# Kernel optimization log

Hardware: AMD Instinct MI355X
Metric: run time of the kernel (lower is better)

The kernel has to match this reference:

```python
import jax, jax.numpy as jnp
import numpy as np

BATCH = 2
TIME_N = 196
SPACE_F = 8
D_MODEL = 768
N_HEADS = 12
D_STATE = 16
DT_RANK = 48  # ceil(768/16)
D_CONV = 4
SEQ = 1 + TIME_N * SPACE_F


def _ln(x, w, b, eps=1e-5):
    m = x.mean(-1, keepdims=True)
    v = ((x - m) ** 2).mean(-1, keepdims=True)
    return (x - m) * jax.lax.rsqrt(v + eps) * w + b


def _silu(x):
    return x * jax.nn.sigmoid(x)


def _causal_conv(x, w, b):
    # x: (B, L, d); depthwise causal conv1d, kernel D_CONV, padding left
    L = x.shape[1]
    xp = jnp.pad(x, ((0, 0), (D_CONV - 1, 0), (0, 0)))
    return sum(xp[:, k:k + L, :] * w[:, k] for k in range(D_CONV)) + b


def _ssm(u, delta, A, Bm, C, Dp):
    # u, delta: (B,L,d); A: (d,N); Bm, C: (B,L,N)
    dA = jnp.exp(delta[..., None] * A)                    # (B,L,d,N)
    dBu = (delta * u)[..., None] * Bm[:, :, None, :]      # (B,L,d,N)
    B, L, d, N = dA.shape

    def step(h, inp):
        a, bu = inp
        h = a * h + bu
        return h, h

    _, hs = jax.lax.scan(step, jnp.zeros((B, d, N), dA.dtype),
                         (dA.transpose(1, 0, 2, 3), dBu.transpose(1, 0, 2, 3)))
    return jnp.einsum('lbdn,bln->bld', hs, C) + u * Dp


def _mamba_dir(xp, z, conv_w, conv_b, xproj_w, dt_w, dt_b, A_log, Dp, flip):
    if flip:
        xp = xp[:, ::-1]
        z = z[:, ::-1]
    xc = _silu(_causal_conv(xp, conv_w, conv_b))
    x_dbl = xc @ xproj_w.T
    dt = x_dbl[..., :DT_RANK]
    Bm = x_dbl[..., DT_RANK:DT_RANK + D_STATE]
    C = x_dbl[..., DT_RANK + D_STATE:]
    delta = jax.nn.softplus(dt @ dt_w.T + dt_b)
    y = _ssm(xc, delta, -jnp.exp(A_log), Bm, C, Dp) * _silu(z)
    if flip:
        y = y[:, ::-1]
    return y


def _mamba(x, in_w, cw, cb, xw, dw, db, Al, Dp, cwb, cbb, xwb, dwb, dbb, Alb, Dpb, out_w):
    # bimamba v2: forward scan + backward (flipped) scan, summed, then out_proj
    xz = x @ in_w.T
    xp, z = jnp.split(xz, 2, axis=-1)
    y = (_mamba_dir(xp, z, cw, cb, xw, dw, db, Al, Dp, False)
         + _mamba_dir(xp, z, cwb, cbb, xwb, dwb, dbb, Alb, Dpb, True))
    return y @ out_w.T


def _mha(x, in_w, in_b, out_w, out_b):
    # torch nn.MultiheadAttention default (batch_first=False):
    # x is (L, N, E); attention runs over dim 0 (L), dim 1 (N) is batch.
    L, N, E = x.shape
    hd = E // N_HEADS
    qkv = x @ in_w.T + in_b
    q, k, v = jnp.split(qkv, 3, axis=-1)
    q = q.reshape(L, N, N_HEADS, hd)
    k = k.reshape(L, N, N_HEADS, hd)
    v = v.reshape(L, N, N_HEADS, hd)
    scores = jnp.einsum('lnhk,mnhk->nhlm', q, k) / jnp.sqrt(jnp.asarray(hd, x.dtype))
    o = jnp.einsum('nhlm,mnhk->lnhk', jax.nn.softmax(scores, axis=-1), v)
    return o.reshape(L, N, E) @ out_w.T + out_b


def _forward(x, norm1_w, norm1_b, norm2_w, norm2_b, norm3_w, norm3_b,
             attn_in_w, attn_in_b, attn_out_w, attn_out_b,
             m_in_w, m_conv_w, m_conv_b, m_xproj_w, m_dt_w, m_dt_b, m_Alog, m_D,
             m_conv_wb, m_conv_bb, m_xproj_wb, m_dt_wb, m_dt_bb, m_Alog_b, m_D_b,
             m_out_w, fc1_w, fc1_b, fc2_w, fc2_b, time_n, space_f):
    b, _, d = x.shape
    init_cls = x[:, :1]
    res_x = x
    # 'b (n t) d -> (b n) t d'
    xt = x[:, 1:].reshape(b, time_n, space_f, d).reshape(b * time_n, space_f, d)
    time_out = _mamba(_ln(xt, norm3_w, norm3_b), m_in_w, m_conv_w, m_conv_b,
                      m_xproj_w, m_dt_w, m_dt_b, m_Alog, m_D,
                      m_conv_wb, m_conv_bb, m_xproj_wb, m_dt_wb, m_dt_bb,
                      m_Alog_b, m_D_b, m_out_w)
    time_res = (xt + time_out).reshape(b, time_n, space_f, d)
    # cls repeat: 'b t d -> (b t) 1 d'
    cls = jnp.repeat(init_cls, space_f, axis=1).reshape(b * space_f, 1, d)
    # 'b (n t) d -> (b t) n d'
    xs = time_res.transpose(0, 2, 1, 3).reshape(b * space_f, time_n, d)
    xs = jnp.concatenate([cls, xs], axis=1)  # (b*t, n+1, d)
    space_out = _mha(_ln(xs, norm1_w, norm1_b), attn_in_w, attn_in_b, attn_out_w, attn_out_b)
    cls_tok = space_out[:, 0].reshape(b, space_f, d).mean(1, keepdims=True)
    # '(b t) n d -> b (n t) d'
    sp = space_out[:, 1:].reshape(b, space_f, time_n, d).transpose(0, 2, 1, 3).reshape(b, time_n * space_f, d)
    x = res_x + jnp.concatenate([cls_tok, sp], axis=1)
    h = _ln(x, norm2_w, norm2_b)
    h = jax.nn.gelu(h @ fc1_w.T + fc1_b, approximate=False) @ fc2_w.T + fc2_b
    return x + h


def setup_inputs():
    ks = iter(jax.random.split(jax.random.key(0), 64))

    def nrm(shape, s=0.02):
        return jax.random.normal(next(ks), shape, dtype=jnp.float32) * s

    d = D_MODEL
    Alog = jnp.log(jnp.tile(jnp.arange(1, D_STATE + 1, dtype=jnp.float32), (d, 1)))
    return dict(
        x=jax.random.normal(next(ks), (BATCH, SEQ, d), dtype=jnp.float32),
        norm1_w=jnp.ones((d,), jnp.float32), norm1_b=jnp.zeros((d,), jnp.float32),
        norm2_w=jnp.ones((d,), jnp.float32), norm2_b=jnp.zeros((d,), jnp.float32),
        norm3_w=jnp.ones((d,), jnp.float32), norm3_b=jnp.zeros((d,), jnp.float32),
        attn_in_w=nrm((3 * d, d)), attn_in_b=nrm((3 * d,)),
        attn_out_w=nrm((d, d)), attn_out_b=nrm((d,)),
        m_in_w=nrm((2 * d, d)),
        m_conv_w=nrm((d, D_CONV), 0.2), m_conv_b=nrm((d,), 0.1),
        m_xproj_w=nrm((DT_RANK + 2 * D_STATE, d)),
        m_dt_w=nrm((d, DT_RANK), 0.1), m_dt_b=nrm((d,), 0.5),
        m_Alog=Alog, m_D=jnp.ones((d,), jnp.float32),
        m_conv_wb=nrm((d, D_CONV), 0.2), m_conv_bb=nrm((d,), 0.1),
        m_xproj_wb=nrm((DT_RANK + 2 * D_STATE, d)),
        m_dt_wb=nrm((d, DT_RANK), 0.1), m_dt_bb=nrm((d,), 0.5),
        m_Alog_b=Alog, m_D_b=jnp.ones((d,), jnp.float32),
        m_out_w=nrm((d, d)),
        fc1_w=nrm((4 * d, d)), fc1_b=nrm((4 * d,), 0.01),
        fc2_w=nrm((d, 4 * d)), fc2_b=nrm((d,), 0.01),
        time_n=TIME_N, space_f=SPACE_F,
    )


def reference(x, norm1_w, norm1_b, norm2_w, norm2_b, norm3_w, norm3_b,
              attn_in_w, attn_in_b, attn_out_w, attn_out_b,
              m_in_w, m_conv_w, m_conv_b, m_xproj_w, m_dt_w, m_dt_b, m_Alog, m_D,
              m_conv_wb, m_conv_bb, m_xproj_wb, m_dt_wb, m_dt_bb, m_Alog_b, m_D_b,
              m_out_w, fc1_w, fc1_b, fc2_w, fc2_b, time_n, space_f):
    return _forward(x, norm1_w, norm1_b, norm2_w, norm2_b, norm3_w, norm3_b,
                    attn_in_w, attn_in_b, attn_out_w, attn_out_b,
                    m_in_w, m_conv_w, m_conv_b, m_xproj_w, m_dt_w, m_dt_b, m_Alog, m_D,
                    m_conv_wb, m_conv_bb, m_xproj_wb, m_dt_wb, m_dt_bb, m_Alog_b, m_D_b,
                    m_out_w, fc1_w, fc1_b, fc2_w, fc2_b, time_n, space_f)
```

## Files before the change

### kernel.cpp

```cpp
#include <hip/hip_runtime.h>
#include <hip/hip_bf16.h>
#include <math.h>

#define DM 768
#define NBATCH 2
#define TIMEN 196
#define SPACEF 8
#define SEQL 1569
#define NSTATE 16
#define MT 3136
#define NSEQ 392
#define AT 3152
#define XTOK 3138

typedef __attribute__((ext_vector_type(8))) short s16x8;
typedef __attribute__((ext_vector_type(4))) float f32x4;
typedef __hip_bfloat16 bf16;

__device__ __forceinline__ float siluf(float x){ return x / (1.0f + expf(-x)); }
__device__ __forceinline__ float silu_fast(float x){ return __fdividef(x, 1.0f + __expf(-x)); }
__device__ __forceinline__ float geluf(float x){ return 0.5f*x*(1.0f + erff(x*0.70710678118654752f)); }
__device__ __forceinline__ float softplusf(float x){ return (x > 20.0f) ? x : log1pf(expf(x)); }
__device__ __forceinline__ int imin(int a, int b){ return a < b ? a : b; }

#define GLD_LDS16(g, l) __builtin_amdgcn_global_load_lds( \
    (const __attribute__((address_space(1))) void*)(g), \
    (__attribute__((address_space(3))) void*)(l), 16, 0, 0)

template<int N, int K, int Np, int Kp>
__device__ __forceinline__ void cvt_seg(const float* __restrict__ src, bf16* __restrict__ dst){
  const int total = Np * Kp;
  int base = blockIdx.x * 1024 + threadIdx.x;
  #pragma unroll
  for (int e = 0; e < 4; e++){
    int idx = base + e * 256;
    if (idx < total){
      int n = idx / Kp, k = idx % Kp;
      float v = (n < N && k < K) ? src[n * K + k] : 0.0f;
      dst[idx] = __float2bfloat16(v);
    }
  }
}

__global__ __launch_bounds__(256) void cvtw_kernel(
    const float* s0, const float* s1, const float* s2, const float* s3,
    const float* s4, const float* s5, const float* s6, const float* s7,
    const float* s8, const float* s9, bf16* w)
{
  switch (blockIdx.y) {
    case 0: cvt_seg<1536,768,1536,768>(s0, w + 0);        break;
    case 1: cvt_seg<  80,768, 128,768>(s1, w + 1179648);  break;
    case 2: cvt_seg<  80,768, 128,768>(s2, w + 1277952);  break;
    case 3: cvt_seg< 768, 48, 768, 64>(s3, w + 1376256);  break;
    case 4: cvt_seg< 768, 48, 768, 64>(s4, w + 1425408);  break;
    case 5: cvt_seg< 768,768, 768,768>(s5, w + 1474560);  break;
    case 6: cvt_seg<2304,768,2304,768>(s6, w + 2064384);  break;
    case 7: cvt_seg< 768,768, 768,768>(s7, w + 3833856);  break;
    case 8: cvt_seg<3072,768,3072,768>(s8, w + 4423680);  break;
    default:cvt_seg< 768,3072,768,3072>(s9, w + 6782976); break;
  }
}

__device__ __forceinline__ float block_sum256(float v, float* sm){
  #pragma unroll
  for (int o = 32; o > 0; o >>= 1) v += __shfl_down(v, o);
  __syncthreads();
  if ((threadIdx.x & 63) == 0) sm[threadIdx.x >> 6] = v;
  __syncthreads();
  return sm[0] + sm[1] + sm[2] + sm[3];
}

__global__ __launch_bounds__(256) void ln_kernel(
    const float* __restrict__ src0, const float* __restrict__ src1,
    const float* __restrict__ w, const float* __restrict__ b,
    bf16* __restrict__ out, int mode)
{
  __shared__ float sm[4];
  int tok = blockIdx.x;
  const float* src;
  if (mode == 0) {
    src = src0 + (size_t)tok * DM;
  } else if (mode == 1) {
    int bi = tok / (TIMEN*SPACEF), r = tok % (TIMEN*SPACEF);
    src = src0 + ((size_t)bi * SEQL + 1 + r) * DM;
  } else {
    int sidx = tok / 197, p = tok % 197;
    if (p == 0) src = src0 + (size_t)(sidx >> 3) * SEQL * DM;
    else { int bi = sidx >> 3, f = sidx & 7, t = p - 1;
           src = src1 + (size_t)((bi*TIMEN + t)*SPACEF + f) * DM; }
  }
  int tid = threadIdx.x;
  float xr[3];
  #pragma unroll
  for (int i = 0; i < 3; i++) xr[i] = src[tid + i*256];
  float mean = block_sum256(xr[0]+xr[1]+xr[2], sm) * (1.0f/768.0f);
  float v0 = xr[0]-mean, v1 = xr[1]-mean, v2 = xr[2]-mean;
  float var = block_sum256(v0*v0 + v1*v1 + v2*v2, sm) * (1.0f/768.0f);
  float rstd = rsqrtf(var + 1e-5f);
  bf16* o = out + (size_t)tok * DM;
  #pragma unroll
  for (int i = 0; i < 3; i++){ int c = tid + i*256;
    o[c] = __float2bfloat16((xr[i]-mean)*rstd*w[c] + b[c]); }
}

template<int BM, int BN>
__global__ __launch_bounds__(256) void mgemm(
    const bf16* __restrict__ A, int lda,
    const bf16* __restrict__ W0, const bf16* __restrict__ W1, int ldw,
    const float* __restrict__ bias0, const float* __restrict__ bias1,
    const float* __restrict__ resid,
    void* __restrict__ Cout, int M, int mhalf, int N, int ldc, int KP,
    int act, int resmode, int outbf16)
{
  constexpr int AG = BM/64;
  constexpr int BG = BN/64;
  constexpr int WM = BM/2, WN = BN/2, MI = WM/16, NJ = WN/16;
  __shared__ bf16 As[2][BM*32];
  __shared__ bf16 Bs[2][BN*32];
  int tid = threadIdx.x;
  int wave = tid >> 6, lane = tid & 63;
  int m0 = blockIdx.y * BM, n0 = blockIdx.x * BN;
  int wr = wave >> 1, wc = wave & 1;

  const bf16* Wt = (m0 < mhalf) ? W0 : W1;
  const float* bias = (m0 < mhalf) ? bias0 : bias1;

  f32x4 acc[MI][NJ];
  #pragma unroll
  for (int i = 0; i < MI; i++)
    #pragma unroll
    for (int j = 0; j < NJ; j++) acc[i][j] = (f32x4){0.f,0.f,0.f,0.f};

  int sr4 = lane >> 2, sc0 = (lane & 3) * 8;
  int lr16 = lane & 15, ks = (lane >> 4) * 8;

  auto stage = [&](int buf, int k0){
    #pragma unroll
    for (int g = 0; g < AG; g++){
      int r = wave*(16*AG) + g*16;
      const bf16* ga = A + (size_t)imin(m0 + r + sr4, M-1)*lda + k0 + sc0;
      GLD_LDS16(ga, &As[buf][r*32]);
    }
    #pragma unroll
    for (int g = 0; g < BG; g++){
      int r = wave*(16*BG) + g*16;
      const bf16* gb = Wt + (size_t)(n0 + r + sr4)*ldw + k0 + sc0;
      GLD_LDS16(gb, &Bs[buf][r*32]);
    }
  };

  auto compute = [&](int buf){
    s16x8 afr[MI], bfr[NJ];
    #pragma unroll
    for (int i = 0; i < MI; i++) afr[i] = *(const s16x8*)&As[buf][(wr*WM + i*16 + lr16)*32 + ks];
    #pragma unroll
    for (int j = 0; j < NJ; j++) bfr[j] = *(const s16x8*)&Bs[buf][(wc*WN + j*16 + lr16)*32 + ks];
    #pragma unroll
    for (int i = 0; i < MI; i++)
      #pragma unroll
      for (int j = 0; j < NJ; j++)
        acc[i][j] = __builtin_amdgcn_mfma_f32_16x16x32_bf16(afr[i], bfr[j], acc[i][j], 0, 0, 0);
  };

  stage(0, 0);
  __syncthreads();
  int cur = 0;
  for (int k0 = 32; k0 < KP; k0 += 32){
    stage(cur ^ 1, k0);
    compute(cur);
    __syncthreads();
    cur ^= 1;
  }
  compute(cur);

  #pragma unroll
  for (int i = 0; i < MI; i++){
    int rowb = m0 + wr*WM + i*16 + (lane >> 4)*4;
    #pragma unroll
    for (int j = 0; j < NJ; j++){
      int col = n0 + wc*WN + j*16 + lr16;
      if (col >= N) continue;
      float bv = bias ? bias[col] : 0.0f;
      #pragma unroll
      for (int r = 0; r < 4; r++){
        int row = rowb + r;
        if (row >= M) continue;
        float v = acc[i][j][r] + bv;
        if (act == 1) v = geluf(v);
        else if (act == 2) v = softplusf(v);
        if (resmode == 1) v += resid[(size_t)row*ldc + col];
        else if (resmode == 2){
          int bi = row / (TIMEN*SPACEF), rr = row % (TIMEN*SPACEF);
          v += resid[((size_t)bi*SEQL + 1 + rr)*DM + col];
        }
        if (outbf16) ((bf16*)Cout)[(size_t)row*ldc + col] = __float2bfloat16(v);
        else         ((float*)Cout)[(size_t)row*ldc + col] = v;
      }
    }
  }
}

__global__ __launch_bounds__(256) void conv_kernel(
    const float* __restrict__ xz,
    const float* __restrict__ wf, const float* __restrict__ bf,
    const float* __restrict__ wb, const float* __restrict__ bb,
    bf16* __restrict__ xcf, bf16* __restrict__ xcb)
{
  int g = blockIdx.x*256 + threadIdx.x;
  if (g >= NSEQ*DM) return;
  int s = g / DM, d = g % DM;
  float xr[8];
  #pragma unroll
  for (int j = 0; j < 8; j++) xr[j] = xz[(size_t)(s*8 + j)*1536 + d];
  float wfv[4], wbv[4];
  #pragma unroll
  for (int k = 0; k < 4; k++){ wfv[k] = wf[d*4+k]; wbv[k] = wb[d*4+k]; }
  float bfv = bf[d], bbv = bb[d];
  #pragma unroll
  for (int l = 0; l < 8; l++) {
    float af = bfv, ab = bbv;
    #pragma unroll
    for (int k = 0; k < 4; k++) {
      if (l + k >= 3) {
        af += wfv[k] * xr[l + k - 3];
        ab += wbv[k] * xr[10 - l - k];
      }
    }
    xcf[(size_t)(s*8 + l)*DM + d] = __float2bfloat16(silu_fast(af));
    xcb[(size_t)(s*8 + l)*DM + d] = __float2bfloat16(silu_fast(ab));
  }
}

__global__ __launch_bounds__(256) void ssm_kernel(
    const float* __restrict__ xz,
    const bf16* __restrict__ xcf, const bf16* __restrict__ xcb,
    const bf16* __restrict__ dblf, const bf16* __restrict__ dblb,
    const bf16* __restrict__ dlf, const bf16* __restrict__ dlb,
    const float* __restrict__ Alogf, const float* __restrict__ Df,
    const float* __restrict__ Alogb, const float* __restrict__ Db,
    bf16* __restrict__ y)
{
  int s = blockIdx.y;
  int d = blockIdx.x*256 + threadIdx.x;
  int tid = threadIdx.x;
  __shared__ float sBC[2][8][32];
  #pragma unroll
  for (int i = 0; i < 2; i++){
    int idx = tid + i*256;
    int dir = idx >> 8, r = idx & 255, l = r >> 5, j = r & 31;
    const bf16* p = dir ? dblb : dblf;
    sBC[dir][l][j] = __bfloat162float(p[(size_t)(s*8 + l)*80 + 48 + j]);
  }
  float Af[NSTATE], Ab[NSTATE];
  #pragma unroll
  for (int n = 0; n < NSTATE; n++) {
    Af[n] = -__expf(Alogf[d*NSTATE + n]);
    Ab[n] = -__expf(Alogb[d*NSTATE + n]);
  }
  float Dfv = Df[d], Dbv = Db[d];
  __syncthreads();

  float hf[NSTATE] = {}, hb[NSTATE] = {};
  float yf[8], yb[8];
  #pragma unroll
  for (int l = 0; l < 8; l++) {
    int t = s*8 + l;
    float delf = __bfloat162float(dlf[(size_t)t*DM + d]);
    float uf   = __bfloat162float(xcf[(size_t)t*DM + d]);
    float duf  = delf * uf;
    float accf = 0.0f;
    #pragma unroll
    for (int n = 0; n < NSTATE; n++) {
      hf[n] = __expf(delf*Af[n])*hf[n] + duf*sBC[0][l][n];
      accf += hf[n]*sBC[0][l][16+n];
    }
    yf[l] = accf + uf*Dfv;
    float delb = __bfloat162float(dlb[(size_t)t*DM + d]);
    float ub   = __bfloat162float(xcb[(size_t)t*DM + d]);
    float dub  = delb * ub;
    float accb = 0.0f;
    #pragma unroll
    for (int n = 0; n < NSTATE; n++) {
      hb[n] = __expf(delb*Ab[n])*hb[n] + dub*sBC[1][l][n];
      accb += hb[n]*sBC[1][l][16+n];
    }
    yb[7-l] = accb + ub*Dbv;
  }
  #pragma unroll
  for (int l = 0; l < 8; l++) {
    int t = s*8 + l;
    float zv = xz[(size_t)t*1536 + DM + d];
    y[(size_t)t*DM + d] = __float2bfloat16((yf[l] + yb[l]) * silu_fast(zv));
  }
}

__global__ __launch_bounds__(256) void attn_kernel(
    const bf16* __restrict__ qkv, bf16* __restrict__ ao)
{
  int n = blockIdx.x / 12, h = blockIdx.x % 12;
  __shared__ float qs[16][65], ks[16][65], vs[16][65], ps[16][17];
  int tid = threadIdx.x;
  for (int e = tid; e < 1024; e += 256) {
    int l = e >> 6, c = e & 63;
    size_t row = ((size_t)l*197 + n)*2304 + h*64 + c;
    qs[l][c] = __bfloat162float(qkv[row]);
    ks[l][c] = __bfloat162float(qkv[row + 768]);
    vs[l][c] = __bfloat162float(qkv[row + 1536]);
  }
  __syncthreads();
  int l = tid >> 4, m = tid & 15;
  float sc = 0.0f;
  #pragma unroll
  for (int c = 0; c < 64; c++) sc += qs[l][c]*ks[m][c];
  sc *= 0.125f;
  float mx = sc;
  #pragma unroll
  for (int o = 8; o > 0; o >>= 1) mx = fmaxf(mx, __shfl_xor(mx, o, 16));
  float p = __expf(sc - mx);
  float smv = p;
  #pragma unroll
  for (int o = 8; o > 0; o >>= 1) smv += __shfl_xor(smv, o, 16);
  ps[l][m] = __fdividef(p, smv);
  __syncthreads();
  for (int e = tid; e < 1024; e += 256) {
    int ll = e >> 6, c = e & 63;
    float acc = 0.0f;
    #pragma unroll
    for (int mm = 0; mm < 16; mm++) acc += ps[ll][mm]*vs[mm][c];
    ao[((size_t)ll*197 + n)*768 + h*64 + c] = __float2bfloat16(acc);
  }
}

__global__ __launch_bounds__(256) void scatter_kernel(
    const float* __restrict__ x, const float* __restrict__ so,
    float* __restrict__ xnew)
{
  int idx = blockIdx.x*256 + threadIdx.x;
  if (idx >= NBATCH*SEQL*DM) return;
  int bi = idx / (SEQL*DM);
  int rem = idx % (SEQL*DM);
  int row = rem / DM, d = rem % DM;
  float v;
  if (row == 0) {
    float acc = 0.0f;
    #pragma unroll
    for (int f = 0; f < SPACEF; f++)
      acc += so[((size_t)(bi*SPACEF + f)*197)*DM + d];
    v = x[idx] + acc * 0.125f;
  } else {
    int t = (row - 1) >> 3, f = (row - 1) & 7;
    v = x[idx] + so[((size_t)(bi*SPACEF + f)*197 + 1 + t)*DM + d];
  }
  xnew[idx] = v;
}

extern "C" void kernel_launch(void* const* d_in, const int* in_sizes, int n_in,
                              void* d_out, int out_size, void* d_ws, size_t ws_size,
                              hipStream_t stream) {
  const float* x        = (const float*)d_in[0];
  const float* norm1_w  = (const float*)d_in[1];
  const float* norm1_b  = (const float*)d_in[2];
  const float* norm2_w  = (const float*)d_in[3];
  const float* norm2_b  = (const float*)d_in[4];
  const float* norm3_w  = (const float*)d_in[5];
  const float* norm3_b  = (const float*)d_in[6];
  const float* attn_in_w  = (const float*)d_in[7];
  const float* attn_in_b  = (const float*)d_in[8];
  const float* attn_out_w = (const float*)d_in[9];
  const float* attn_out_b = (const float*)d_in[10];
  const float* m_in_w   = (const float*)d_in[11];
  const float* m_conv_w = (const float*)d_in[12];
  const float* m_conv_b = (const float*)d_in[13];
  const float* m_xproj_w= (const float*)d_in[14];
  const float* m_dt_w   = (const float*)d_in[15];
  const float* m_dt_b   = (const float*)d_in[16];
  const float* m_Alog   = (const float*)d_in[17];
  const float* m_D      = (const float*)d_in[18];
  const float* m_conv_wb= (const float*)d_in[19];
  const float* m_conv_bb= (const float*)d_in[20];
  const float* m_xproj_wb=(const float*)d_in[21];
  const float* m_dt_wb  = (const float*)d_in[22];
  const float* m_dt_bb  = (const float*)d_in[23];
  const float* m_Alog_b = (const float*)d_in[24];
  const float* m_D_b    = (const float*)d_in[25];
  const float* m_out_w  = (const float*)d_in[26];
  const float* fc1_w    = (const float*)d_in[27];
  const float* fc1_b    = (const float*)d_in[28];
  const float* fc2_w    = (const float*)d_in[29];
  const float* fc2_b    = (const float*)d_in[30];

  char* wsb = (char*)d_ws;
  bf16*  wpool  = (bf16*)(wsb + 0);
  bf16*  ln3    = (bf16*)(wsb + 18284544);
  float* xz     = (float*)(wsb + 23101440);
  bf16*  xcf    = (bf16*)(wsb + 42369024);
  bf16*  xcb    = (bf16*)(wsb + 47185920);
  bf16*  dblf   = (bf16*)(wsb + 52002816);
  bf16*  dblb   = (bf16*)(wsb + 52504576);
  bf16*  dlf    = (bf16*)(wsb + 53006336);
  bf16*  dlb    = (bf16*)(wsb + 57823232);
  bf16*  y      = ln3;
  float* tres   = (float*)(wsb + 62640128);
  bf16*  xsln   = (bf16*)(wsb + 23101440);
  float* so     = (float*)(wsb + 27942912);
  bf16*  qkv    = (bf16*)(wsb + 42369024);
  bf16*  ao     = (bf16*)(wsb + 56893440);
  float* xnew   = tres;
  bf16*  ln2o   = (bf16*)(wsb + 23101440);
  bf16*  h1     = (bf16*)(wsb + 42369024);

  bf16* w_in  = wpool + 0;
  bf16* w_xpf = wpool + 1179648;
  bf16* w_xpb = wpool + 1277952;
  bf16* w_dtf = wpool + 1376256;
  bf16* w_dtb = wpool + 1425408;
  bf16* w_out = wpool + 1474560;
  bf16* w_qkv = wpool + 2064384;
  bf16* w_ao  = wpool + 3833856;
  bf16* w_fc1 = wpool + 4423680;
  bf16* w_fc2 = wpool + 6782976;

  const int BIGM = 1 << 30;

  cvtw_kernel<<<dim3(2304, 10), 256, 0, stream>>>(
      m_in_w, m_xproj_w, m_xproj_wb, m_dt_w, m_dt_wb, m_out_w,
      attn_in_w, attn_out_w, fc1_w, fc2_w, wpool);

  ln_kernel<<<MT, 256, 0, stream>>>(x, nullptr, norm3_w, norm3_b, ln3, 1);
  mgemm<128,64><<<dim3(24, 25), 256, 0, stream>>>(ln3, DM, w_in, w_in, DM,
      nullptr, nullptr, nullptr, xz, MT, BIGM, 1536, 1536, DM, 0, 0, 0);
  conv_kernel<<<(NSEQ*DM + 255)/256, 256, 0, stream>>>(
      xz, m_conv_w, m_conv_b, m_conv_wb, m_conv_bb, xcf, xcb);
  mgemm<64,64><<<dim3(2, 98), 256, 0, stream>>>(xcf, DM, w_xpf, w_xpb, DM,
      nullptr, nullptr, nullptr, dblf, 2*MT, MT, 80, 80, DM, 0, 0, 1);
  mgemm<64,64><<<dim3(12, 98), 256, 0, stream>>>(dblf, 80, w_dtf, w_dtb, 64,
      m_dt_b, m_dt_bb, nullptr, dlf, 2*MT, MT, DM, DM, 64, 2, 0, 1);
  ssm_kernel<<<dim3(3, NSEQ), 256, 0, stream>>>(
      xz, xcf, xcb, dblf, dblb, dlf, dlb, m_Alog, m_D, m_Alog_b, m_D_b, y);
  mgemm<64,64><<<dim3(12, 49), 256, 0, stream>>>(y, DM, w_out, w_out, DM,
      nullptr, nullptr, x, tres, MT, BIGM, DM, DM, DM, 0, 2, 0);

  ln_kernel<<<AT, 256, 0, stream>>>(x, tres, norm1_w, norm1_b, xsln, 2);
  mgemm<128,64><<<dim3(36, 25), 256, 0, stream>>>(xsln, DM, w_qkv, w_qkv, DM,
      attn_in_b, attn_in_b, nullptr, qkv, AT, BIGM, 2304, 2304, DM, 0, 0, 1);
  attn_kernel<<<197*12, 256, 0, stream>>>(qkv, ao);
  mgemm<64,64><<<dim3(12, 50), 256, 0, stream>>>(ao, DM, w_ao, w_ao, DM,
      attn_out_b, attn_out_b, nullptr, so, AT, BIGM, DM, DM, DM, 0, 0, 0);
  scatter_kernel<<<(NBATCH*SEQL*DM + 255)/256, 256, 0, stream>>>(x, so, xnew);

  ln_kernel<<<XTOK, 256, 0, stream>>>(xnew, nullptr, norm2_w, norm2_b, ln2o, 0);
  mgemm<128,64><<<dim3(48, 25), 256, 0, stream>>>(ln2o, DM, w_fc1, w_fc1, DM,
      fc1_b, fc1_b, nullptr, h1, XTOK, BIGM, 3072, 3072, DM, 1, 0, 1);
  mgemm<64,64><<<dim3(12, 50), 256, 0, stream>>>(h1, 3072, w_fc2, w_fc2, 3072,
      fc2_b, fc2_b, xnew, (float*)d_out, XTOK, BIGM, DM, DM, 3072, 0, 1, 0);
}
```

Measured before the change: 318.9 us.

## Triple-buffer GEMM k-loop with vmcnt waits and XCD-aware block remapping

The bf16 MFMA GEMM moves from a double-buffered LDS pipeline with full __syncthreads to a three-stage ring. It waits with explicit s_waitcnt vmcnt counts and a single barrier per iteration, so two tiles are in flight while the current one is computed. It also remaps block IDs so consecutive workgroups on the same XCD get contiguous tiles, which should improve L2 reuse. The cost is 50% more LDS per block, which may reduce occupancy, and the hand-tuned vmcnt values depend on how many loads are issued per stage.

```diff
diff --git a/kernel.cpp b/kernel.cpp
--- a/kernel.cpp
+++ b/kernel.cpp
@@ -17,7 +17,6 @@
 typedef __attribute__((ext_vector_type(4))) float f32x4;
 typedef __hip_bfloat16 bf16;
 
-__device__ __forceinline__ float siluf(float x){ return x / (1.0f + expf(-x)); }
 __device__ __forceinline__ float silu_fast(float x){ return __fdividef(x, 1.0f + __expf(-x)); }
 __device__ __forceinline__ float geluf(float x){ return 0.5f*x*(1.0f + erff(x*0.70710678118654752f)); }
 __device__ __forceinline__ float softplusf(float x){ return (x > 20.0f) ? x : log1pf(expf(x)); }
@@ -114,12 +113,20 @@
 {
   constexpr int AG = BM/64;
   constexpr int BG = BN/64;
+  constexpr int L  = AG + BG;
   constexpr int WM = BM/2, WN = BN/2, MI = WM/16, NJ = WN/16;
-  __shared__ bf16 As[2][BM*32];
-  __shared__ bf16 Bs[2][BN*32];
+  __shared__ bf16 As[3][BM*32];
+  __shared__ bf16 Bs[3][BN*32];
   int tid = threadIdx.x;
   int wave = tid >> 6, lane = tid & 63;
-  int m0 = blockIdx.y * BM, n0 = blockIdx.x * BN;
+
+  int nwg = gridDim.x * gridDim.y;
+  int bid = blockIdx.y * gridDim.x + blockIdx.x;
+  int q = nwg >> 3, r = nwg & 7;
+  int xcd = bid & 7, lidx = bid >> 3;
+  int wg = (xcd < r ? xcd*(q+1) : r*(q+1) + (xcd-r)*q) + lidx;
+  int m0 = (wg / gridDim.x) * BM, n0 = (wg % gridDim.x) * BN;
+
   int wr = wave >> 1, wc = wave & 1;
 
   const bf16* Wt = (m0 < mhalf) ? W0 : W1;
@@ -137,15 +144,15 @@
   auto stage = [&](int buf, int k0){
     #pragma unroll
     for (int g = 0; g < AG; g++){
-      int r = wave*(16*AG) + g*16;
-      const bf16* ga = A + (size_t)imin(m0 + r + sr4, M-1)*lda + k0 + sc0;
-      GLD_LDS16(ga, &As[buf][r*32]);
+      int rr = wave*(16*AG) + g*16;
+      const bf16* ga = A + (size_t)imin(m0 + rr + sr4, M-1)*lda + k0 + sc0;
+      GLD_LDS16(ga, &As[buf][rr*32]);
     }
     #pragma unroll
     for (int g = 0; g < BG; g++){
-      int r = wave*(16*BG) + g*16;
-      const bf16* gb = Wt + (size_t)(n0 + r + sr4)*ldw + k0 + sc0;
-      GLD_LDS16(gb, &Bs[buf][r*32]);
+      int rr = wave*(16*BG) + g*16;
+      const bf16* gb = Wt + (size_t)(n0 + rr + sr4)*ldw + k0 + sc0;
+      GLD_LDS16(gb, &Bs[buf][rr*32]);
     }
   };
 
@@ -162,16 +169,22 @@
         acc[i][j] = __builtin_amdgcn_mfma_f32_16x16x32_bf16(afr[i], bfr[j], acc[i][j], 0, 0, 0);
   };
 
+  int nk = KP >> 5;
   stage(0, 0);
-  __syncthreads();
-  int cur = 0;
-  for (int k0 = 32; k0 < KP; k0 += 32){
-    stage(cur ^ 1, k0);
-    compute(cur);
-    __syncthreads();
-    cur ^= 1;
-  }
-  compute(cur);
+  if (nk > 1) stage(1, 32);
+  int k = 0;
+  for (; k < nk - 1; ++k){
+    if constexpr (L == 2) asm volatile("s_waitcnt vmcnt(2)" ::: "memory");
+    else                  asm volatile("s_waitcnt vmcnt(3)" ::: "memory");
+    __builtin_amdgcn_s_barrier();
+    __builtin_amdgcn_sched_barrier(0);
+    if (k + 2 < nk) stage((k+2)%3, (k+2)*32);
+    compute(k%3);
+  }
+  asm volatile("s_waitcnt vmcnt(0)" ::: "memory");
+  __builtin_amdgcn_s_barrier();
+  __builtin_amdgcn_sched_barrier(0);
+  compute(k%3);
 
   #pragma unroll
   for (int i = 0; i < MI; i++){
@@ -182,10 +195,10 @@
       if (col >= N) continue;
       float bv = bias ? bias[col] : 0.0f;
       #pragma unroll
-      for (int r = 0; r < 4; r++){
-        int row = rowb + r;
+      for (int r2 = 0; r2 < 4; r2++){
+        int row = rowb + r2;
         if (row >= M) continue;
-        float v = acc[i][j][r] + bv;
+        float v = acc[i][j][r2] + bv;
         if (act == 1) v = geluf(v);
         else if (act == 2) v = softplusf(v);
         if (resmode == 1) v += resid[(size_t)row*ldc + col];
```

New measurement: 330.0 us. 1.03x slower.

## Add split-K with reduction kernel, XCD-aware block remap, smaller GEMM tiles

Applied to the files above, without the earlier changes.

Adds a split-K mode to the GEMM: the grid's z dimension partitions K, partial fp32 results go to scratch buffers, and a new reduction kernel sums them and applies bias and residual. It is used for the three N=768 GEMMs (out_proj, attn out, fc2). Block IDs are also remapped so consecutive tiles land on the same XCD for better L2 reuse. The large GEMMs switch from 128x64 to 64x64 tiles to get more workgroups. Split-K adds extra partial-sum traffic and a kernel launch, and the buffer aliasing is reworked to hold the partials.

```diff
diff --git a/kernel.cpp b/kernel.cpp
--- a/kernel.cpp
+++ b/kernel.cpp
@@ -17,7 +17,6 @@
 typedef __attribute__((ext_vector_type(4))) float f32x4;
 typedef __hip_bfloat16 bf16;
 
-__device__ __forceinline__ float siluf(float x){ return x / (1.0f + expf(-x)); }
 __device__ __forceinline__ float silu_fast(float x){ return __fdividef(x, 1.0f + __expf(-x)); }
 __device__ __forceinline__ float geluf(float x){ return 0.5f*x*(1.0f + erff(x*0.70710678118654752f)); }
 __device__ __forceinline__ float softplusf(float x){ return (x > 20.0f) ? x : log1pf(expf(x)); }
@@ -110,7 +109,7 @@
     const float* __restrict__ bias0, const float* __restrict__ bias1,
     const float* __restrict__ resid,
     void* __restrict__ Cout, int M, int mhalf, int N, int ldc, int KP,
-    int act, int resmode, int outbf16)
+    int act, int resmode, int outbf16, int skw)
 {
   constexpr int AG = BM/64;
   constexpr int BG = BN/64;
@@ -119,10 +118,19 @@
   __shared__ bf16 Bs[2][BN*32];
   int tid = threadIdx.x;
   int wave = tid >> 6, lane = tid & 63;
-  int m0 = blockIdx.y * BM, n0 = blockIdx.x * BN;
+
+  int nwg = gridDim.x * gridDim.y;
+  int bid = blockIdx.y * gridDim.x + blockIdx.x;
+  int q = nwg >> 3, r = nwg & 7;
+  int xcd = bid & 7, lidx = bid >> 3;
+  int wg = (xcd < r ? xcd*(q+1) : r*(q+1) + (xcd-r)*q) + lidx;
+  int m0 = (wg / gridDim.x) * BM, n0 = (wg % gridDim.x) * BN;
+
   int wr = wave >> 1, wc = wave & 1;
 
-  const bf16* Wt = (m0 < mhalf) ? W0 : W1;
+  int koff = blockIdx.z * KP;
+  const bf16* Ak = A + koff;
+  const bf16* Wt = ((m0 < mhalf) ? W0 : W1) + koff;
   const float* bias = (m0 < mhalf) ? bias0 : bias1;
 
   f32x4 acc[MI][NJ];
@@ -137,15 +145,15 @@
   auto stage = [&](int buf, int k0){
     #pragma unroll
     for (int g = 0; g < AG; g++){
-      int r = wave*(16*AG) + g*16;
-      const bf16* ga = A + (size_t)imin(m0 + r + sr4, M-1)*lda + k0 + sc0;
-      GLD_LDS16(ga, &As[buf][r*32]);
+      int rr = wave*(16*AG) + g*16;
+      const bf16* ga = Ak + (size_t)imin(m0 + rr + sr4, M-1)*lda + k0 + sc0;
+      GLD_LDS16(ga, &As[buf][rr*32]);
     }
     #pragma unroll
     for (int g = 0; g < BG; g++){
-      int r = wave*(16*BG) + g*16;
-      const bf16* gb = Wt + (size_t)(n0 + r + sr4)*ldw + k0 + sc0;
-      GLD_LDS16(gb, &Bs[buf][r*32]);
+      int rr = wave*(16*BG) + g*16;
+      const bf16* gb = Wt + (size_t)(n0 + rr + sr4)*ldw + k0 + sc0;
+      GLD_LDS16(gb, &Bs[buf][rr*32]);
     }
   };
 
@@ -182,10 +190,15 @@
       if (col >= N) continue;
       float bv = bias ? bias[col] : 0.0f;
       #pragma unroll
-      for (int r = 0; r < 4; r++){
-        int row = rowb + r;
+      for (int r2 = 0; r2 < 4; r2++){
+        int row = rowb + r2;
         if (row >= M) continue;
-        float v = acc[i][j][r] + bv;
+        float v = acc[i][j][r2];
+        if (skw > 1){
+          ((float*)Cout)[((size_t)(blockIdx.z*M) + row)*ldc + col] = v;
+          continue;
+        }
+        v += bv;
         if (act == 1) v = geluf(v);
         else if (act == 2) v = softplusf(v);
         if (resmode == 1) v += resid[(size_t)row*ldc + col];
@@ -198,6 +211,36 @@
       }
     }
   }
+}
+
+__global__ __launch_bounds__(256) void redk(
+    const float* __restrict__ part, const float* __restrict__ bias,
+    const float* __restrict__ resid, float* __restrict__ out,
+    int M, int sk, int resmode)
+{
+  int i = blockIdx.x*256 + threadIdx.x;
+  if (i*4 >= M*768) return;
+  int row = i / 192;
+  int c4 = (i - row*192) * 4;
+  size_t base = (size_t)row*768 + c4;
+  float4 v = *(const float4*)(part + base);
+  for (int z = 1; z < sk; z++){
+    float4 p = *(const float4*)(part + (size_t)z*M*768 + base);
+    v.x += p.x; v.y += p.y; v.z += p.z; v.w += p.w;
+  }
+  if (bias){
+    float4 b = *(const float4*)(bias + c4);
+    v.x += b.x; v.y += b.y; v.z += b.z; v.w += b.w;
+  }
+  if (resmode == 1){
+    float4 r = *(const float4*)(resid + base);
+    v.x += r.x; v.y += r.y; v.z += r.z; v.w += r.w;
+  } else if (resmode == 2){
+    int bi = row / (TIMEN*SPACEF), rr = row % (TIMEN*SPACEF);
+    float4 r = *(const float4*)(resid + ((size_t)bi*SEQL + 1 + rr)*DM + c4);
+    v.x += r.x; v.y += r.y; v.z += r.z; v.w += r.w;
+  }
+  *(float4*)(out + base) = v;
 }
 
 __global__ __launch_bounds__(256) void conv_kernel(
@@ -401,13 +444,16 @@
   bf16*  dlb    = (bf16*)(wsb + 57823232);
   bf16*  y      = ln3;
   float* tres   = (float*)(wsb + 62640128);
+  float* part1  = (float*)(wsb + 23101440);
   bf16*  xsln   = (bf16*)(wsb + 23101440);
   float* so     = (float*)(wsb + 27942912);
   bf16*  qkv    = (bf16*)(wsb + 42369024);
-  bf16*  ao     = (bf16*)(wsb + 56893440);
+  bf16*  ao     = (bf16*)(wsb + 18284544);
+  float* part2  = (float*)(wsb + 42369024);
   float* xnew   = tres;
   bf16*  ln2o   = (bf16*)(wsb + 23101440);
   bf16*  h1     = (bf16*)(wsb + 42369024);
+  float* part3  = (float*)(wsb + 18284544);
 
   bf16* w_in  = wpool + 0;
   bf16* w_xpf = wpool + 1179648;
@@ -427,30 +473,33 @@
       attn_in_w, attn_out_w, fc1_w, fc2_w, wpool);
 
   ln_kernel<<<MT, 256, 0, stream>>>(x, nullptr, norm3_w, norm3_b, ln3, 1);
-  mgemm<128,64><<<dim3(24, 25), 256, 0, stream>>>(ln3, DM, w_in, w_in, DM,
-      nullptr, nullptr, nullptr, xz, MT, BIGM, 1536, 1536, DM, 0, 0, 0);
+  mgemm<64,64><<<dim3(24, 49), 256, 0, stream>>>(ln3, DM, w_in, w_in, DM,
+      nullptr, nullptr, nullptr, xz, MT, BIGM, 1536, 1536, DM, 0, 0, 0, 1);
   conv_kernel<<<(NSEQ*DM + 255)/256, 256, 0, stream>>>(
       xz, m_conv_w, m_conv_b, m_conv_wb, m_conv_bb, xcf, xcb);
   mgemm<64,64><<<dim3(2, 98), 256, 0, stream>>>(xcf, DM, w_xpf, w_xpb, DM,
-      nullptr, nullptr, nullptr, dblf, 2*MT, MT, 80, 80, DM, 0, 0, 1);
+      nullptr, nullptr, nullptr, dblf, 2*MT, MT, 80, 80, DM, 0, 0, 1, 1);
   mgemm<64,64><<<dim3(12, 98), 256, 0, stream>>>(dblf, 80, w_dtf, w_dtb, 64,
-      m_dt_b, m_dt_bb, nullptr, dlf, 2*MT, MT, DM, DM, 64, 2, 0, 1);
+      m_dt_b, m_dt_bb, nullptr, dlf, 2*MT, MT, DM, DM, 64, 2, 0, 1, 1);
   ssm_kernel<<<dim3(3, NSEQ), 256, 0, stream>>>(
       xz, xcf, xcb, dblf, dblb, dlf, dlb, m_Alog, m_D, m_Alog_b, m_D_b, y);
-  mgemm<64,64><<<dim3(12, 49), 256, 0, stream>>>(y, DM, w_out, w_out, DM,
-      nullptr, nullptr, x, tres, MT, BIGM, DM, DM, DM, 0, 2, 0);
+  mgemm<64,64><<<dim3(12, 49, 2), 256, 0, stream>>>(y, DM, w_out, w_out, DM,
+      nullptr, nullptr, nullptr, part1, MT, BIGM, DM, DM, 384, 0, 0, 0, 2);
+  redk<<<2352, 256, 0, stream>>>(part1, nullptr, x, tres, MT, 2, 2);
 
   ln_kernel<<<AT, 256, 0, stream>>>(x, tres, norm1_w, norm1_b, xsln, 2);
-  mgemm<128,64><<<dim3(36, 25), 256, 0, stream>>>(xsln, DM, w_qkv, w_qkv, DM,
-      attn_in_b, attn_in_b, nullptr, qkv, AT, BIGM, 2304, 2304, DM, 0, 0, 1);
+  mgemm<64,64><<<dim3(36, 50), 256, 0, stream>>>(xsln, DM, w_qkv, w_qkv, DM,
+      attn_in_b, attn_in_b, nullptr, qkv, AT, BIGM, 2304, 2304, DM, 0, 0, 1, 1);
   attn_kernel<<<197*12, 256, 0, stream>>>(qkv, ao);
-  mgemm<64,64><<<dim3(12, 50), 256, 0, stream>>>(ao, DM, w_ao, w_ao, DM,
-      attn_out_b, attn_out_b, nullptr, so, AT, BIGM, DM, DM, DM, 0, 0, 0);
+  mgemm<64,64><<<dim3(12, 50, 2), 256, 0, stream>>>(ao, DM, w_ao, w_ao, DM,
+      nullptr, nullptr, nullptr, part2, AT, BIGM, DM, DM, 384, 0, 0, 0, 2);
+  redk<<<2364, 256, 0, stream>>>(part2, attn_out_b, nullptr, so, AT, 2, 0);
   scatter_kernel<<<(NBATCH*SEQL*DM + 255)/256, 256, 0, stream>>>(x, so, xnew);
 
   ln_kernel<<<XTOK, 256, 0, stream>>>(xnew, nullptr, norm2_w, norm2_b, ln2o, 0);
-  mgemm<128,64><<<dim3(48, 25), 256, 0, stream>>>(ln2o, DM, w_fc1, w_fc1, DM,
-      fc1_b, fc1_b, nullptr, h1, XTOK, BIGM, 3072, 3072, DM, 1, 0, 1);
-  mgemm<64,64><<<dim3(12, 50), 256, 0, stream>>>(h1, 3072, w_fc2, w_fc2, 3072,
-      fc2_b, fc2_b, xnew, (float*)d_out, XTOK, BIGM, DM, DM, 3072, 0, 1, 0);
-}
+  mgemm<64,64><<<dim3(48, 50), 256, 0, stream>>>(ln2o, DM, w_fc1, w_fc1, DM,
+      fc1_b, fc1_b, nullptr, h1, XTOK, BIGM, 3072, 3072, DM, 1, 0, 1, 1);
+  mgemm<64,64><<<dim3(12, 50, 2), 256, 0, stream>>>(h1, 3072, w_fc2, w_fc2, 3072,
+      nullptr, nullptr, nullptr, part3, XTOK, BIGM, DM, DM, 1536, 0, 0, 0, 2);
+  redk<<<2354, 256, 0, stream>>>(part3, fc2_b, xnew, (float*)d_out, XTOK, 2, 1);
+}
```

After: 315.6 us. About the same (-1.0%).
